# Performance work log

Measured on AMD Instinct MI355X. Metric: run time of the kernel, lower is better.

Reference implementation:

```python
import jax, jax.numpy as jnp
import numpy as np

B, S, D, H = 2, 2048, 2048, 16
HD = D // H  # head_dim = 128


def setup_inputs() -> dict:
    key = jax.random.key(0)
    ks = jax.random.split(key, 10)
    sc = 1.0 / np.sqrt(D)
    inp = {
        "hidden_states": jax.random.normal(ks[0], (B, S, D), dtype=jnp.float32),
        "attention_mask": jnp.zeros((B, 1, S, S), dtype=jnp.float32),
        "Wq": jax.random.normal(ks[1], (D, D), dtype=jnp.float32) * sc,
        "bq": jnp.zeros((D,), dtype=jnp.float32),
        "Wk": jax.random.normal(ks[2], (D, D), dtype=jnp.float32) * sc,
        "bk": jnp.zeros((D,), dtype=jnp.float32),
        "Wv": jax.random.normal(ks[3], (D, D), dtype=jnp.float32) * sc,
        "bv": jnp.zeros((D,), dtype=jnp.float32),
        "Wo": jax.random.normal(ks[4], (D, D), dtype=jnp.float32) * sc,
        "bo": jnp.zeros((D,), dtype=jnp.float32),
    }
    return inp


def reference(hidden_states, attention_mask, Wq, bq, Wk, bk, Wv, bv, Wo, bo):
    # torch Linear: y = x @ W^T + b
    q = hidden_states @ Wq.T + bq
    k = hidden_states @ Wk.T + bk
    v = hidden_states @ Wv.T + bv
    # [B,S,D] -> [B,H,S,HD]
    q = q.reshape(B, S, H, HD).transpose(0, 2, 1, 3)
    k = k.reshape(B, S, H, HD).transpose(0, 2, 1, 3)
    v = v.reshape(B, S, H, HD).transpose(0, 2, 1, 3)
    # RoPE in source is an identity passthrough; apply_rotary_pos_emb returns (q, k) unchanged.
    scores = jnp.einsum("bhqd,bhkd->bhqk", q, k) / jnp.sqrt(jnp.float32(HD))
    scores = scores + attention_mask  # broadcast over heads
    attn = jax.nn.softmax(scores, axis=-1)
    out = jnp.einsum("bhqk,bhkd->bhqd", attn, v)
    out = out.transpose(0, 2, 1, 3).reshape(B, S, D)
    return out @ Wo.T + bo
```

## Files before the change

### kernel.cpp

```cpp
#include <hip/hip_runtime.h>
#include <hip/hip_bf16.h>
#include <math.h>

typedef unsigned short u16;
typedef unsigned int u32;
typedef __attribute__((ext_vector_type(8))) short bf16x8;
typedef __attribute__((ext_vector_type(4))) float f32x4;

constexpr int Bc = 2, Sc = 2048, Dc = 2048, Hc = 16, HDc = 128;
constexpr int Mc = Bc * Sc;
constexpr float SCALE = 0.08838834764831845f;

__device__ inline u16 f2bf(float f) {
  __hip_bfloat16 h = __float2bfloat16(f);
  return __builtin_bit_cast(u16, h);
}

typedef const __attribute__((address_space(1))) u32 glb_u32;
typedef __attribute__((address_space(3))) u32 lds_u32;
__device__ inline void gload16(const void* g, void* l) {
  __builtin_amdgcn_global_load_lds((glb_u32*)g, (lds_u32*)l, 16, 0, 0);
}

__global__ __launch_bounds__(256) void cvt5(
    const float* __restrict__ s0, u16* __restrict__ d0, int n0,
    const float* __restrict__ s1, u16* __restrict__ d1, int n1,
    const float* __restrict__ s2, u16* __restrict__ d2, int n2,
    const float* __restrict__ s3, u16* __restrict__ d3, int n3,
    const float* __restrict__ s4, u16* __restrict__ d4, int n4) {
  int i = blockIdx.x * 256 + threadIdx.x;
  const float* s; u16* d;
  if (i < n0) { s = s0; d = d0; }
  else { i -= n0;
    if (i < n1) { s = s1; d = d1; }
    else { i -= n1;
      if (i < n2) { s = s2; d = d2; }
      else { i -= n2;
        if (i < n3) { s = s3; d = d3; }
        else { i -= n3;
          if (i >= n4) return;
          s = s4; d = d4; } } } }
  float4 v = reinterpret_cast<const float4*>(s)[i];
  ushort4 o;
  o.x = f2bf(v.x); o.y = f2bf(v.y); o.z = f2bf(v.z); o.w = f2bf(v.w);
  reinterpret_cast<ushort4*>(d)[i] = o;
}

constexpr int GBM = 128, GBN = 128, GBK = 64;

template <int MODE>
__global__ __launch_bounds__(256) void gemm_bf16(
    const u16* __restrict__ A, const u16* __restrict__ W,
    const float* __restrict__ bias, void* __restrict__ outp, float scale) {
  __shared__ u16 smem[17408];
  u16* As = smem;
  u16* Bs = smem + 8192;
  char* Asb = (char*)As;
  char* Bsb = (char*)Bs;
  const int t = threadIdx.x;
  const int w = t >> 6, lane = t & 63, g = lane >> 4, c = lane & 15;
  const int wm = w >> 1, wn = w & 1;
  const int m0 = blockIdx.y * GBM, n0 = blockIdx.x * GBN;

  f32x4 acc[4][4];
#pragma unroll
  for (int m = 0; m < 4; ++m)
#pragma unroll
    for (int n = 0; n < 4; ++n) acc[m][n] = 0.f;

  for (int k0 = 0; k0 < Dc; k0 += GBK) {
#pragma unroll
    for (int i = 0; i < 4; ++i) {
      int u = i * 256 + t;
      int row = u >> 3, cu = u & 7;
      int ub = i * 256 + (t & 192);
      gload16(A + (size_t)(m0 + row) * Dc + k0 + cu * 8, Asb + ub * 16);
      gload16(W + (size_t)(n0 + row) * Dc + k0 + cu * 8, Bsb + ub * 16);
    }
    __syncthreads();
#pragma unroll
    for (int s = 0; s < 2; ++s) {
      bf16x8 af[4], bfv[4];
#pragma unroll
      for (int m = 0; m < 4; ++m)
        af[m] = *(const bf16x8*)(Asb + (wm * 64 + m * 16 + c) * 128 + s * 64 + g * 16);
#pragma unroll
      for (int n = 0; n < 4; ++n)
        bfv[n] = *(const bf16x8*)(Bsb + (wn * 64 + n * 16 + c) * 128 + s * 64 + g * 16);
#pragma unroll
      for (int m = 0; m < 4; ++m)
#pragma unroll
        for (int n = 0; n < 4; ++n)
          acc[m][n] = __builtin_amdgcn_mfma_f32_16x16x32_bf16(af[m], bfv[n], acc[m][n], 0, 0, 0);
    }
    __syncthreads();
  }

  if (MODE == 2) {
    u16* CT = smem;
    __syncthreads();
#pragma unroll
    for (int m = 0; m < 4; ++m)
#pragma unroll
      for (int n = 0; n < 4; ++n) {
        int lcol = wn * 64 + n * 16 + c;
        float bv = bias[n0 + lcol];
#pragma unroll
        for (int r = 0; r < 4; ++r) {
          int lrow = wm * 64 + m * 16 + g * 4 + r;
          CT[lcol * 136 + lrow] = f2bf(acc[m][n][r] + bv);
        }
      }
    __syncthreads();
    const int b = m0 >> 11, h = n0 >> 7, s0 = m0 & (Sc - 1);
    u16* op = (u16*)outp;
#pragma unroll
    for (int i = 0; i < 8; ++i) {
      int u = i * 256 + t;
      int d = u >> 4, su = u & 15;
      size_t gbase = ((size_t)((b * Hc + h) * HDc) + d) * Sc + s0;
#pragma unroll
      for (int p2 = 0; p2 < 4; ++p2) {
        int sl = su * 8 + p2 * 2;
        u32 val = (u32)CT[d * 136 + sl] | ((u32)CT[d * 136 + sl + 1] << 16);
        int w6 = sl & 63, blk = sl >> 6;
        int slot = ((w6 >> 5) << 5) | (((w6 >> 2) & 3) << 3) |
                   (((w6 >> 4) & 1) << 2) | (w6 & 3);
        *(u32*)&op[gbase + blk * 64 + slot] = val;
      }
    }
    return;
  }

#pragma unroll
  for (int m = 0; m < 4; ++m)
#pragma unroll
    for (int n = 0; n < 4; ++n) {
      int col = n0 + wn * 64 + n * 16 + c;
      float bv = bias[col];
#pragma unroll
      for (int r = 0; r < 4; ++r) {
        int row = m0 + wm * 64 + m * 16 + g * 4 + r;
        float v = (acc[m][n][r] + bv) * scale;
        if (MODE == 0) {
          int b = row >> 11, si = row & (Sc - 1);
          int h = col >> 7, d = col & (HDc - 1);
          ((u16*)outp)[((size_t)((b * Hc + h) * Sc + si)) * HDc + d] = f2bf(v);
        } else {
          ((float*)outp)[(size_t)row * Dc + col] = v;
        }
      }
    }
}

__global__ __launch_bounds__(256, 4) void attn_mfma(
    const u16* __restrict__ Q, const u16* __restrict__ K,
    const u16* __restrict__ VT, const float* __restrict__ mask,
    u16* __restrict__ outb) {
  __shared__ u16 Ks[64 * 128];
  __shared__ u16 Vt[128 * 64];
  char* Ksb = (char*)Ks;
  char* Vtb = (char*)Vt;
  const int t = threadIdx.x, w = t >> 6, lane = t & 63, g = lane >> 4, c = lane & 15;
  const int bid = blockIdx.x;
  const int nid = (bid & 7) * 128 + (bid >> 3);
  const int bh = nid >> 5;
  const int q0 = (nid & 31) * 64;
  const int bq = bh >> 4, h = bh & 15;
  const u16* Qp = Q + ((size_t)bh << 18);
  const u16* Kp = K + ((size_t)bh << 18);
  const u16* VTp = VT + ((size_t)bh << 18);

  bf16x8 qf[4];
  {
    int qr = q0 + w * 16 + c;
#pragma unroll
    for (int d0 = 0; d0 < 4; ++d0)
      qf[d0] = *(const bf16x8*)(Qp + (size_t)qr * HDc + d0 * 32 + g * 8);
  }

  f32x4 po[8];
#pragma unroll
  for (int m = 0; m < 8; ++m) po[m] = 0.f;
  float lsum = 0.f;
  const float* mrow = mask + ((size_t)bq * Sc + q0 + w * 16 + c) * Sc;

#pragma unroll 1
  for (int kt = 0; kt < 32; ++kt) {
    const int k0 = kt * 64;
#pragma unroll
    for (int i = 0; i < 4; ++i) {
      int u = i * 256 + t, row = u >> 4, p = u & 15;
      int cu = (p & 8) | ((p ^ row) & 7);
      gload16(Kp + (size_t)(k0 + row) * HDc + cu * 8,
              Ksb + (i * 256 + (t & 192)) * 16);
    }
#pragma unroll
    for (int i = 0; i < 4; ++i) {
      int u = i * 256 + t, d = u >> 3, p = u & 7;
      int cu = (p ^ d) & 7;
      gload16(VTp + (size_t)d * Sc + k0 + cu * 8,
              Vtb + (i * 256 + (t & 192)) * 16);
    }
    float4 mk[4];
#pragma unroll
    for (int n = 0; n < 4; ++n)
      mk[n] = *(const float4*)(mrow + k0 + n * 16 + g * 4);
    __syncthreads();

    f32x4 sfr[4];
#pragma unroll
    for (int n = 0; n < 4; ++n) sfr[n] = 0.f;
    __builtin_amdgcn_s_setprio(1);
#pragma unroll
    for (int ds = 0; ds < 4; ++ds)
#pragma unroll
      for (int n = 0; n < 4; ++n) {
        int row = n * 16 + c;
        int cu = ds * 4 + g;
        int scu = (cu & 8) | ((cu ^ row) & 7);
        bf16x8 kf = *(const bf16x8*)(Ksb + row * 256 + scu * 16);
        sfr[n] = __builtin_amdgcn_mfma_f32_16x16x32_bf16(kf, qf[ds], sfr[n], 0, 0, 0);
      }
    __builtin_amdgcn_s_setprio(0);

    u32 w01[4], w23[4];
#pragma unroll
    for (int n = 0; n < 4; ++n) {
      float p0 = __expf(sfr[n][0] + mk[n].x);
      float p1 = __expf(sfr[n][1] + mk[n].y);
      float p2 = __expf(sfr[n][2] + mk[n].z);
      float p3 = __expf(sfr[n][3] + mk[n].w);
      lsum += (p0 + p1) + (p2 + p3);
      w01[n] = (u32)f2bf(p0) | ((u32)f2bf(p1) << 16);
      w23[n] = (u32)f2bf(p2) | ((u32)f2bf(p3) << 16);
    }

    __builtin_amdgcn_s_setprio(1);
#pragma unroll
    for (int s2 = 0; s2 < 2; ++s2) {
      uint4 pw;
      pw.x = w01[s2 * 2];
      pw.y = w23[s2 * 2];
      pw.z = w01[s2 * 2 + 1];
      pw.w = w23[s2 * 2 + 1];
      bf16x8 pf = __builtin_bit_cast(bf16x8, pw);
#pragma unroll
      for (int m = 0; m < 8; ++m) {
        int d = m * 16 + c;
        int scuv = ((s2 * 4 + g) ^ (d & 7)) & 7;
        bf16x8 vf = *(const bf16x8*)(Vtb + d * 128 + scuv * 16);
        po[m] = __builtin_amdgcn_mfma_f32_16x16x32_bf16(vf, pf, po[m], 0, 0, 0);
      }
    }
    __builtin_amdgcn_s_setprio(0);
    __syncthreads();
  }

  lsum += __shfl_xor(lsum, 16, 64);
  lsum += __shfl_xor(lsum, 32, 64);
  const float rlq = 1.0f / lsum;
  const int qg = q0 + w * 16 + c;
  u16* obase = outb + ((size_t)(bq * Sc + qg)) * Dc + h * HDc;
#pragma unroll
  for (int m = 0; m < 8; ++m) {
    ushort4 o4;
    o4.x = f2bf(po[m][0] * rlq);
    o4.y = f2bf(po[m][1] * rlq);
    o4.z = f2bf(po[m][2] * rlq);
    o4.w = f2bf(po[m][3] * rlq);
    *(ushort4*)(obase + m * 16 + g * 4) = o4;
  }
}

extern "C" void kernel_launch(void* const* d_in, const int* in_sizes, int n_in,
                              void* d_out, int out_size, void* d_ws,
                              size_t ws_size, hipStream_t stream) {
  const float* hs   = (const float*)d_in[0];
  const float* mask = (const float*)d_in[1];
  const float* Wq   = (const float*)d_in[2];
  const float* bqp  = (const float*)d_in[3];
  const float* Wk   = (const float*)d_in[4];
  const float* bkp  = (const float*)d_in[5];
  const float* Wv   = (const float*)d_in[6];
  const float* bvp  = (const float*)d_in[7];
  const float* Wo   = (const float*)d_in[8];
  const float* bop  = (const float*)d_in[9];

  u16* Xb  = (u16*)d_ws;
  u16* Wqb = Xb + (size_t)Mc * Dc;
  u16* Wkb = Wqb + (size_t)Dc * Dc;
  u16* Wvb = Wkb + (size_t)Dc * Dc;
  u16* Wob = Wvb + (size_t)Dc * Dc;
  u16* qb  = Wob + (size_t)Dc * Dc;
  u16* kb  = qb + (size_t)Mc * Dc;
  u16* vtb = kb + (size_t)Mc * Dc;
  u16* ab  = vtb + (size_t)Mc * Dc;

  const int nh4 = Mc * Dc / 4;
  const int nw4 = Dc * Dc / 4;
  cvt5<<<dim3((nh4 + 4 * nw4) / 256), dim3(256), 0, stream>>>(
      hs, Xb, nh4, Wq, Wqb, nw4, Wk, Wkb, nw4, Wv, Wvb, nw4, Wo, Wob, nw4);

  dim3 blk(256);
  dim3 gg(Dc / GBN, Mc / GBM);
  gemm_bf16<0><<<gg, blk, 0, stream>>>(Xb, Wqb, bqp, qb, SCALE);
  gemm_bf16<0><<<gg, blk, 0, stream>>>(Xb, Wkb, bkp, kb, 1.0f);
  gemm_bf16<2><<<gg, blk, 0, stream>>>(Xb, Wvb, bvp, vtb, 1.0f);
  attn_mfma<<<dim3(1024), blk, 0, stream>>>(qb, kb, vtb, mask, ab);
  gemm_bf16<1><<<gg, blk, 0, stream>>>(ab, Wob, bop, d_out, 1.0f);
}
```

Baseline: 344.9 us.

## Process two 16-row query tiles per wave with 128-thread attention blocks

```diff
diff --git a/kernel.cpp b/kernel.cpp
--- a/kernel.cpp
+++ b/kernel.cpp
@@ -153,7 +153,7 @@
     }
 }
 
-__global__ __launch_bounds__(256, 4) void attn_mfma(
+__global__ __launch_bounds__(128, 2) void attn_mfma(
     const u16* __restrict__ Q, const u16* __restrict__ K,
     const u16* __restrict__ VT, const float* __restrict__ mask,
     u16* __restrict__ outb) {
@@ -171,46 +171,52 @@
   const u16* Kp = K + ((size_t)bh << 18);
   const u16* VTp = VT + ((size_t)bh << 18);
 
-  bf16x8 qf[4];
+  bf16x8 qf0[4], qf1[4];
   {
-    int qr = q0 + w * 16 + c;
-#pragma unroll
-    for (int d0 = 0; d0 < 4; ++d0)
-      qf[d0] = *(const bf16x8*)(Qp + (size_t)qr * HDc + d0 * 32 + g * 8);
-  }
-
-  f32x4 po[8];
-#pragma unroll
-  for (int m = 0; m < 8; ++m) po[m] = 0.f;
-  float lsum = 0.f;
-  const float* mrow = mask + ((size_t)bq * Sc + q0 + w * 16 + c) * Sc;
+    int qr0 = q0 + w * 32 + c;
+    int qr1 = qr0 + 16;
+#pragma unroll
+    for (int d0 = 0; d0 < 4; ++d0) {
+      qf0[d0] = *(const bf16x8*)(Qp + (size_t)qr0 * HDc + d0 * 32 + g * 8);
+      qf1[d0] = *(const bf16x8*)(Qp + (size_t)qr1 * HDc + d0 * 32 + g * 8);
+    }
+  }
+
+  f32x4 po0[8], po1[8];
+#pragma unroll
+  for (int m = 0; m < 8; ++m) { po0[m] = 0.f; po1[m] = 0.f; }
+  float lsum0 = 0.f, lsum1 = 0.f;
+  const float* mrow0 = mask + ((size_t)bq * Sc + q0 + w * 32 + c) * Sc;
+  const float* mrow1 = mrow0 + (size_t)16 * Sc;
 
 #pragma unroll 1
   for (int kt = 0; kt < 32; ++kt) {
     const int k0 = kt * 64;
 #pragma unroll
-    for (int i = 0; i < 4; ++i) {
-      int u = i * 256 + t, row = u >> 4, p = u & 15;
+    for (int i = 0; i < 8; ++i) {
+      int u = i * 128 + t, row = u >> 4, p = u & 15;
       int cu = (p & 8) | ((p ^ row) & 7);
       gload16(Kp + (size_t)(k0 + row) * HDc + cu * 8,
-              Ksb + (i * 256 + (t & 192)) * 16);
-    }
-#pragma unroll
-    for (int i = 0; i < 4; ++i) {
-      int u = i * 256 + t, d = u >> 3, p = u & 7;
+              Ksb + (i * 128 + (t & 64)) * 16);
+    }
+#pragma unroll
+    for (int i = 0; i < 8; ++i) {
+      int u = i * 128 + t, d = u >> 3, p = u & 7;
       int cu = (p ^ d) & 7;
       gload16(VTp + (size_t)d * Sc + k0 + cu * 8,
-              Vtb + (i * 256 + (t & 192)) * 16);
-    }
-    float4 mk[4];
-#pragma unroll
-    for (int n = 0; n < 4; ++n)
-      mk[n] = *(const float4*)(mrow + k0 + n * 16 + g * 4);
-    __syncthreads();
-
-    f32x4 sfr[4];
-#pragma unroll
-    for (int n = 0; n < 4; ++n) sfr[n] = 0.f;
+              Vtb + (i * 128 + (t & 64)) * 16);
+    }
+    float4 mk0[4], mk1[4];
+#pragma unroll
+    for (int n = 0; n < 4; ++n) {
+      mk0[n] = *(const float4*)(mrow0 + k0 + n * 16 + g * 4);
+      mk1[n] = *(const float4*)(mrow1 + k0 + n * 16 + g * 4);
+    }
+    __syncthreads();
+
+    f32x4 sfr0[4], sfr1[4];
+#pragma unroll
+    for (int n = 0; n < 4; ++n) { sfr0[n] = 0.f; sfr1[n] = 0.f; }
     __builtin_amdgcn_s_setprio(1);
 #pragma unroll
     for (int ds = 0; ds < 4; ++ds)
@@ -220,56 +226,76 @@
         int cu = ds * 4 + g;
         int scu = (cu & 8) | ((cu ^ row) & 7);
         bf16x8 kf = *(const bf16x8*)(Ksb + row * 256 + scu * 16);
-        sfr[n] = __builtin_amdgcn_mfma_f32_16x16x32_bf16(kf, qf[ds], sfr[n], 0, 0, 0);
+        sfr0[n] = __builtin_amdgcn_mfma_f32_16x16x32_bf16(kf, qf0[ds], sfr0[n], 0, 0, 0);
+        sfr1[n] = __builtin_amdgcn_mfma_f32_16x16x32_bf16(kf, qf1[ds], sfr1[n], 0, 0, 0);
       }
     __builtin_amdgcn_s_setprio(0);
 
-    u32 w01[4], w23[4];
+    u32 a01[4], a23[4], b01[4], b23[4];
 #pragma unroll
     for (int n = 0; n < 4; ++n) {
-      float p0 = __expf(sfr[n][0] + mk[n].x);
-      float p1 = __expf(sfr[n][1] + mk[n].y);
-      float p2 = __expf(sfr[n][2] + mk[n].z);
-      float p3 = __expf(sfr[n][3] + mk[n].w);
-      lsum += (p0 + p1) + (p2 + p3);
-      w01[n] = (u32)f2bf(p0) | ((u32)f2bf(p1) << 16);
-      w23[n] = (u32)f2bf(p2) | ((u32)f2bf(p3) << 16);
+      float p0 = __expf(sfr0[n][0] + mk0[n].x);
+      float p1 = __expf(sfr0[n][1] + mk0[n].y);
+      float p2 = __expf(sfr0[n][2] + mk0[n].z);
+      float p3 = __expf(sfr0[n][3] + mk0[n].w);
+      lsum0 += (p0 + p1) + (p2 + p3);
+      a01[n] = (u32)f2bf(p0) | ((u32)f2bf(p1) << 16);
+      a23[n] = (u32)f2bf(p2) | ((u32)f2bf(p3) << 16);
+      float r0 = __expf(sfr1[n][0] + mk1[n].x);
+      float r1 = __expf(sfr1[n][1] + mk1[n].y);
+      float r2 = __expf(sfr1[n][2] + mk1[n].z);
+      float r3 = __expf(sfr1[n][3] + mk1[n].w);
+      lsum1 += (r0 + r1) + (r2 + r3);
+      b01[n] = (u32)f2bf(r0) | ((u32)f2bf(r1) << 16);
+      b23[n] = (u32)f2bf(r2) | ((u32)f2bf(r3) << 16);
     }
 
     __builtin_amdgcn_s_setprio(1);
 #pragma unroll
     for (int s2 = 0; s2 < 2; ++s2) {
-      uint4 pw;
-      pw.x = w01[s2 * 2];
-      pw.y = w23[s2 * 2];
-      pw.z = w01[s2 * 2 + 1];
-      pw.w = w23[s2 * 2 + 1];
-      bf16x8 pf = __builtin_bit_cast(bf16x8, pw);
+      uint4 pw0, pw1;
+      pw0.x = a01[s2 * 2]; pw0.y = a23[s2 * 2];
+      pw0.z = a01[s2 * 2 + 1]; pw0.w = a23[s2 * 2 + 1];
+      pw1.x = b01[s2 * 2]; pw1.y = b23[s2 * 2];
+      pw1.z = b01[s2 * 2 + 1]; pw1.w = b23[s2 * 2 + 1];
+      bf16x8 pf0 = __builtin_bit_cast(bf16x8, pw0);
+      bf16x8 pf1 = __builtin_bit_cast(bf16x8, pw1);
 #pragma unroll
       for (int m = 0; m < 8; ++m) {
         int d = m * 16 + c;
         int scuv = ((s2 * 4 + g) ^ (d & 7)) & 7;
         bf16x8 vf = *(const bf16x8*)(Vtb + d * 128 + scuv * 16);
-        po[m] = __builtin_amdgcn_mfma_f32_16x16x32_bf16(vf, pf, po[m], 0, 0, 0);
+        po0[m] = __builtin_amdgcn_mfma_f32_16x16x32_bf16(vf, pf0, po0[m], 0, 0, 0);
+        po1[m] = __builtin_amdgcn_mfma_f32_16x16x32_bf16(vf, pf1, po1[m], 0, 0, 0);
       }
     }
     __builtin_amdgcn_s_setprio(0);
     __syncthreads();
   }
 
-  lsum += __shfl_xor(lsum, 16, 64);
-  lsum += __shfl_xor(lsum, 32, 64);
-  const float rlq = 1.0f / lsum;
-  const int qg = q0 + w * 16 + c;
-  u16* obase = outb + ((size_t)(bq * Sc + qg)) * Dc + h * HDc;
+  lsum0 += __shfl_xor(lsum0, 16, 64);
+  lsum0 += __shfl_xor(lsum0, 32, 64);
+  lsum1 += __shfl_xor(lsum1, 16, 64);
+  lsum1 += __shfl_xor(lsum1, 32, 64);
+  const float rl0 = 1.0f / lsum0;
+  const float rl1 = 1.0f / lsum1;
+  const int qg0 = q0 + w * 32 + c;
+  u16* ob0 = outb + ((size_t)(bq * Sc + qg0)) * Dc + h * HDc;
+  u16* ob1 = ob0 + (size_t)16 * Dc;
 #pragma unroll
   for (int m = 0; m < 8; ++m) {
     ushort4 o4;
-    o4.x = f2bf(po[m][0] * rlq);
-    o4.y = f2bf(po[m][1] * rlq);
-    o4.z = f2bf(po[m][2] * rlq);
-    o4.w = f2bf(po[m][3] * rlq);
-    *(ushort4*)(obase + m * 16 + g * 4) = o4;
+    o4.x = f2bf(po0[m][0] * rl0);
+    o4.y = f2bf(po0[m][1] * rl0);
+    o4.z = f2bf(po0[m][2] * rl0);
+    o4.w = f2bf(po0[m][3] * rl0);
+    *(ushort4*)(ob0 + m * 16 + g * 4) = o4;
+    ushort4 o5;
+    o5.x = f2bf(po1[m][0] * rl1);
+    o5.y = f2bf(po1[m][1] * rl1);
+    o5.z = f2bf(po1[m][2] * rl1);
+    o5.w = f2bf(po1[m][3] * rl1);
+    *(ushort4*)(ob1 + m * 16 + g * 4) = o5;
   }
 }
 
@@ -307,6 +333,6 @@
   gemm_bf16<0><<<gg, blk, 0, stream>>>(Xb, Wqb, bqp, qb, SCALE);
   gemm_bf16<0><<<gg, blk, 0, stream>>>(Xb, Wkb, bkp, kb, 1.0f);
   gemm_bf16<2><<<gg, blk, 0, stream>>>(Xb, Wvb, bvp, vtb, 1.0f);
-  attn_mfma<<<dim3(1024), blk, 0, stream>>>(qb, kb, vtb, mask, ab);
+  attn_mfma<<<dim3(1024), dim3(128), 0, stream>>>(qb, kb, vtb, mask, ab);
   gemm_bf16<1><<<gg, blk, 0, stream>>>(ab, Wob, bop, d_out, 1.0f);
 }
```

New measurement: 324.0 us. 6.0% less time.
